# Kernel optimization log

Hardware: AMD Instinct MI355X
Metric: run time of the kernel (lower is better)

Reference implementation:

```python
import jax, jax.numpy as jnp
import numpy as np

N_NODES = 20000
N_EDGES = 160000
FEAT = 512
HEADS = 4
NEG_SLOPE = 0.2


def setup_inputs() -> dict:
    key = jax.random.key(0)
    ks = jax.random.split(key, 8)
    s = 1.0 / np.sqrt(FEAT)
    return {
        "x": jax.random.normal(ks[0], (N_NODES, FEAT), dtype=jnp.float32),
        "edge_index": jax.random.randint(ks[1], (2, N_EDGES), 0, N_NODES, dtype=jnp.int32),
        "W_l": jax.random.normal(ks[2], (FEAT, HEADS * FEAT), dtype=jnp.float32) * s,
        "W_r": jax.random.normal(ks[3], (FEAT, HEADS * FEAT), dtype=jnp.float32) * s,
        "att": jax.random.normal(ks[4], (HEADS, FEAT), dtype=jnp.float32) * s,
        "bias": jax.random.normal(ks[5], (FEAT,), dtype=jnp.float32) * 0.01,
        "W_cls": jax.random.normal(ks[6], (FEAT, 2), dtype=jnp.float32) * s,
        "b_cls": jnp.zeros((2,), dtype=jnp.float32),
    }


def reference(x, edge_index, W_l, W_r, att, bias, W_cls, b_cls):
    N = x.shape[0]
    H, C = att.shape
    # PyG GATv2Conv default: add self-loops
    loops = jnp.arange(N, dtype=edge_index.dtype)
    ei = jnp.concatenate([edge_index, jnp.stack([loops, loops])], axis=1)
    src, dst = ei[0], ei[1]  # message j -> i

    xl = (x @ W_l).reshape(N, H, C)  # source transform
    xr = (x @ W_r).reshape(N, H, C)  # target transform

    # GATv2 score: e_ij = att . LeakyReLU(xl_j + xr_i)   -> [E, H]
    u = xl[src] + xr[dst]                      # [E, H, C]
    e = jnp.einsum('ehc,hc->eh', jax.nn.leaky_relu(u, NEG_SLOPE), att)

    # segment softmax over incoming edges of each dst node
    m = jax.ops.segment_max(e, dst, num_segments=N)          # [N, H]
    alpha = jnp.exp(e - m[dst])
    denom = jax.ops.segment_sum(alpha, dst, num_segments=N)  # [N, H]
    alpha = alpha / denom[dst]

    # aggregate: out_i = sum_j alpha_ij * xl_j
    out = jax.ops.segment_sum(alpha[:, :, None] * xl[src], dst, num_segments=N)  # [N,H,C]
    out = out.mean(axis=1) + bias  # concat=False -> mean over heads, then bias

    return out @ W_cls + b_cls  # [N, num_classes]
```

## Files before the change

kernel.cpp:

```cpp
#include <hip/hip_runtime.h>
#include <hip/hip_bf16.h>

#define FEAT    512
#define HEADS   4
#define NEG     0.2f

typedef unsigned int uint;
typedef unsigned short ushort_t;
typedef __attribute__((ext_vector_type(8))) short bf16x8v;
typedef __attribute__((ext_vector_type(4))) float f32x4v;
typedef __attribute__((ext_vector_type(2))) float f32x2v;
typedef __attribute__((ext_vector_type(4))) uint uint4v;
typedef __attribute__((address_space(3))) uint lds_u32_t;
typedef __attribute__((address_space(1))) const uint g_u32_t;

__device__ inline float bf2f(ushort_t h) { return __uint_as_float(((uint)h) << 16); }
__device__ inline ushort_t f2bf(float f) {
    uint u = __float_as_uint(f);
    u += 0x7fff + ((u >> 16) & 1);
    return (ushort_t)(u >> 16);
}
__device__ inline f32x2v pk_add(f32x2v a, f32x2v b) {
    f32x2v d; asm("v_pk_add_f32 %0, %1, %2" : "=v"(d) : "v"(a), "v"(b)); return d;
}
__device__ inline f32x2v pk_fma(f32x2v a, f32x2v b, f32x2v c) {
    f32x2v d; asm("v_pk_fma_f32 %0, %1, %2, %3" : "=v"(d) : "v"(a), "v"(b), "v"(c)); return d;
}
__device__ inline f32x2v up2v(uint d) {
    f32x2v r; r.x = __uint_as_float(d << 16); r.y = __uint_as_float(d & 0xffff0000u); return r;
}
__device__ inline f32x2v pk_min0(f32x2v a) {
    f32x2v r; r.x = fminf(a.x, 0.f); r.y = fminf(a.y, 0.f); return r;
}

__global__ __launch_bounds__(256) void prep_kernel(
    const ushort_t* __restrict__ xprobe, int* flag,
    int* __restrict__ deg, int N, int NBZ,
    const void* a0, ushort_t* o0, int n0, const void* a1, ushort_t* o1, int n1,
    const void* a2, ushort_t* o2, int n2, const void* a3, ushort_t* o3, int n3,
    const void* __restrict__ Wl, const void* __restrict__ Wr,
    ushort_t* __restrict__ WtL, ushort_t* __restrict__ WtR, int Kk, int HCk) {
    __shared__ int s_isbf;
    __shared__ ushort_t t[64][72];
    int tid = threadIdx.x;
    if (tid < 64) {
        int hits = 0;
        for (int i = tid; i < 128; i += 64) {
            ushort_t w = xprobe[2 * i];
            uint hb = (w >> 8) & 0x7f;
            hits += (hb >= 0x38 && hb <= 0x42) ? 1 : 0;
        }
        #pragma unroll
        for (int off = 32; off >= 1; off >>= 1) hits += __shfl_xor(hits, off);
        if (tid == 0) s_isbf = (hits >= 64) ? 1 : 0;
    }
    __syncthreads();
    int isbf = s_isbf;
    int b = blockIdx.x;
    if (b == 0 && tid == 0) *flag = isbf;

    if (b < NBZ) {
        int i0 = (b * 256 + tid) * 4;
        if (i0 + 4 <= N) *(int4*)&deg[i0] = make_int4(0, 0, 0, 0);
        else for (int j = 0; j < 4; ++j) if (i0 + j < N) deg[i0 + j] = 0;
        return;
    }
    if (b < NBZ + 15) {
        int idx = (b - NBZ) * 256 + tid;
        const void* srcs[4] = {a0, a1, a2, a3};
        ushort_t* dsts[4] = {o0, o1, o2, o3};
        int ns[4] = {n0, n1, n2, n3};
        #pragma unroll
        for (int k = 0; k < 4; ++k) {
            if (idx < ns[k]) {
                dsts[k][idx] = isbf ? ((const ushort_t*)srcs[k])[idx]
                                    : f2bf(((const float*)srcs[k])[idx]);
                return;
            }
            idx -= ns[k];
        }
        return;
    }
    int b2 = b - (NBZ + 15);
    int z = b2 & 1;
    int rest = b2 >> 1;
    int ntk = Kk >> 6;
    int ky = rest % ntk, nxt = rest / ntk;
    const void* in = z ? Wr : Wl;
    ushort_t* outp = z ? WtR : WtL;
    int kt0 = ky * 64, nt0 = nxt * 64;
    int r = tid >> 3;
    int c = (tid & 7) * 8;
    #pragma unroll
    for (int p = 0; p < 2; ++p) {
        int row = r + p * 32;
        size_t base = (size_t)(kt0 + row) * HCk + nt0 + c;
        if (isbf) {
            *(uint4*)&t[row][c] = *(const uint4*)((const ushort_t*)in + base);
        } else {
            const float* f = (const float*)in + base;
            float4 a = *(const float4*)f, bb = *(const float4*)(f + 4);
            ushort_t o[8] = {f2bf(a.x), f2bf(a.y), f2bf(a.z), f2bf(a.w),
                             f2bf(bb.x), f2bf(bb.y), f2bf(bb.z), f2bf(bb.w)};
            *(uint4*)&t[row][c] = *(uint4*)o;
        }
    }
    __syncthreads();
    #pragma unroll
    for (int p = 0; p < 2; ++p) {
        int row = r + p * 32;
        #pragma unroll
        for (int j = 0; j < 8; ++j)
            outp[(size_t)(nt0 + row) * Kk + kt0 + c + j] = t[c + j][row];
    }
}

__global__ __launch_bounds__(256) void histx_kernel(
    const ushort_t* __restrict__ xprobe,
    const int* __restrict__ dstE, int* deg, int E, int NH, int Ngr,
    const void* __restrict__ xin, ushort_t* __restrict__ xc, long long nx) {
    int tid = threadIdx.x;
    int b = blockIdx.x;
    if (b < NH) {
        int i = b * 256 + tid;
        if (i < E) {
            int d = dstE[i];
            if ((uint)d < (uint)Ngr) atomicAdd(&deg[d], 1);
        }
        return;
    }
    __shared__ int s_isbf;
    if (tid < 64) {
        int hits = 0;
        for (int i = tid; i < 128; i += 64) {
            ushort_t w = xprobe[2 * i];
            uint hb = (w >> 8) & 0x7f;
            hits += (hb >= 0x38 && hb <= 0x42) ? 1 : 0;
        }
        #pragma unroll
        for (int off = 32; off >= 1; off >>= 1) hits += __shfl_xor(hits, off);
        if (tid == 0) s_isbf = (hits >= 64) ? 1 : 0;
    }
    __syncthreads();
    if (s_isbf) return;
    long long i0 = ((long long)(b - NH) * 256 + tid) * 8;
    if (i0 + 8 <= nx) {
        const float* f = (const float*)xin + i0;
        float4 a = *(const float4*)f, bb = *(const float4*)(f + 4);
        ushort_t o[8] = {f2bf(a.x), f2bf(a.y), f2bf(a.z), f2bf(a.w),
                         f2bf(bb.x), f2bf(bb.y), f2bf(bb.z), f2bf(bb.w)};
        *(uint4*)&xc[i0] = *(uint4*)o;
    } else {
        for (long long i = i0; i < nx; ++i) xc[i] = f2bf(((const float*)xin)[i]);
    }
}

__global__ __launch_bounds__(256) void scan1(const int* __restrict__ deg, int* __restrict__ part,
                                             int* __restrict__ bsum, int N) {
    __shared__ int tmp[256];
    int b = blockIdx.x, tid = threadIdx.x;
    int i0 = b * 1024 + tid * 4;
    int v[4] = {0, 0, 0, 0};
    if (i0 + 4 <= N) { int4 q = *(const int4*)&deg[i0]; v[0]=q.x+1; v[1]=q.y+1; v[2]=q.z+1; v[3]=q.w+1; }
    else { for (int j = 0; j < 4; ++j) v[j] = (i0 + j < N) ? deg[i0 + j] + 1 : 0; }
    int s0 = v[0], s1 = s0 + v[1], s2 = s1 + v[2], s3 = s2 + v[3];
    tmp[tid] = s3;
    __syncthreads();
    for (int off = 1; off < 256; off <<= 1) {
        int t = (tid >= off) ? tmp[tid - off] : 0;
        __syncthreads();
        tmp[tid] += t;
        __syncthreads();
    }
    int base = tid ? tmp[tid - 1] : 0;
    int e[4] = {base, base + s0, base + s1, base + s2};
    if (i0 + 4 <= N) { *(int4*)&part[i0] = make_int4(e[0], e[1], e[2], e[3]); }
    else { for (int j = 0; j < 4; ++j) if (i0 + j < N) part[i0 + j] = e[j]; }
    if (tid == 255) bsum[b] = tmp[255];
}

__global__ __launch_bounds__(256) void scan3(const int* __restrict__ part, const int* __restrict__ bsum,
                                             int* __restrict__ offsets, int* __restrict__ cursor,
                                             int N, int Nb) {
    __shared__ int s_add, s_tot;
    int b = blockIdx.x, tid = threadIdx.x;
    if (tid < 64) {
        int v = (tid < Nb) ? bsum[tid] : 0;
        int incl = v;
        #pragma unroll
        for (int off = 1; off < 64; off <<= 1) {
            int t = __shfl_up(incl, off);
            if (tid >= off) incl += t;
        }
        if (tid == b) s_add = incl - v;
        if (tid == Nb - 1) s_tot = incl;
    }
    __syncthreads();
    int add = s_add;
    int i0 = b * 1024 + tid * 4;
    #pragma unroll
    for (int j = 0; j < 4; ++j) {
        int i = i0 + j;
        if (i < N) { int o = part[i] + add; offsets[i] = o; cursor[i] = o; }
    }
    if (b == Nb - 1 && tid == 0) offsets[N] = s_tot;
}

__global__ void scatter_kernel(const int* __restrict__ src, const int* __restrict__ dst,
                               int* cursor, int* srcs, int E, int N) {
    int i = blockIdx.x * blockDim.x + threadIdx.x;
    if (i >= E + N) return;
    int s, d;
    if (i < E) { s = src[i]; d = dst[i]; }
    else       { s = i - E; d = i - E; }
    if ((uint)d >= (uint)N) return;
    int pos = atomicAdd(&cursor[d], 1);
    if ((uint)pos < (uint)(E + N)) srcs[pos] = s;
}

__global__ __launch_bounds__(256) void gemm128(const ushort_t* A_bf, const ushort_t* A_cv,
                                               const int* __restrict__ flag,
                                               const ushort_t* __restrict__ Bt,
                                               ushort_t* __restrict__ C,
                                               int M, int Nn, int K, int gyGemm,
                                               const int* __restrict__ esrc,
                                               const int* __restrict__ edst,
                                               int* cursor, int* srcsOut,
                                               int E, int Ngr, int nScB) {
    if ((int)blockIdx.y >= gyGemm) {
        int id = ((int)blockIdx.y - gyGemm) * (int)gridDim.x + (int)blockIdx.x;
        if (id < nScB) {
            int i = id * 256 + (int)threadIdx.x;
            int EN = E + Ngr;
            if (i < EN) {
                int s, d;
                if (i < E) { s = esrc[i]; d = edst[i]; }
                else       { s = i - E; d = i - E; }
                if ((uint)d < (uint)Ngr) {
                    int pos = atomicAdd(&cursor[d], 1);
                    if ((uint)pos < (uint)EN) srcsOut[pos] = s;
                }
            }
        }
        return;
    }
    constexpr int CSTR = 132;
    __shared__ ushort_t SH[128 * CSTR];
    ushort_t* As = SH;
    ushort_t* Bs = SH + 8192;
    const ushort_t* A = (*flag) ? A_bf : A_cv;
    int tid = threadIdx.x;
    int wave = tid >> 6, lane = tid & 63;
    int row0 = blockIdx.y * 128, col0 = blockIdx.x * 128;
    int wm = (wave >> 1) * 64, wn = (wave & 1) * 64;

    f32x4v acc[4][4];
    #pragma unroll
    for (int i = 0; i < 4; ++i)
        #pragma unroll
        for (int j = 0; j < 4; ++j) acc[i][j] = (f32x4v){0.f, 0.f, 0.f, 0.f};

    int fm = lane & 15, kq8 = (lane >> 4) * 8;

    const ushort_t* srcA[2]; ushort_t* dstA0[2]; ushort_t* dstA1[2];
    const ushort_t* srcB[2]; ushort_t* dstB0[2]; ushort_t* dstB1[2];
    #pragma unroll
    for (int i = 0; i < 2; ++i) {
        int p = (wave * 2 + i) * 64 + lane;
        int row = p >> 2, kp = p & 3;
        int gra = row0 + row; if (gra >= M) gra = M - 1;
        srcA[i] = &A[(size_t)gra * K + kp * 8];
        srcB[i] = &Bt[(size_t)(col0 + row) * K + kp * 8];
        dstA0[i] = &As[p * 8]; dstA1[i] = &As[4096 + p * 8];
        dstB0[i] = &Bs[p * 8]; dstB1[i] = &Bs[4096 + p * 8];
    }

    for (int k0 = 0; k0 < K; k0 += 64) {
        #pragma unroll
        for (int i = 0; i < 2; ++i) {
            __builtin_amdgcn_global_load_lds((g_u32_t*)srcA[i],        (lds_u32_t*)dstA0[i], 16, 0, 0);
            __builtin_amdgcn_global_load_lds((g_u32_t*)(srcA[i] + 32), (lds_u32_t*)dstA1[i], 16, 0, 0);
            __builtin_amdgcn_global_load_lds((g_u32_t*)srcB[i],        (lds_u32_t*)dstB0[i], 16, 0, 0);
            __builtin_amdgcn_global_load_lds((g_u32_t*)(srcB[i] + 32), (lds_u32_t*)dstB1[i], 16, 0, 0);
            srcA[i] += 64; srcB[i] += 64;
        }
        __syncthreads();

        #pragma unroll
        for (int panel = 0; panel < 2; ++panel) {
            bf16x8v af[4], bfr[4];
            #pragma unroll
            for (int mi = 0; mi < 4; ++mi)
                af[mi] = *(const bf16x8v*)&As[panel * 4096 + (wm + mi * 16 + fm) * 32 + kq8];
            #pragma unroll
            for (int nj = 0; nj < 4; ++nj)
                bfr[nj] = *(const bf16x8v*)&Bs[panel * 4096 + (wn + nj * 16 + fm) * 32 + kq8];
            #pragma unroll
            for (int mi = 0; mi < 4; ++mi)
                #pragma unroll
                for (int nj = 0; nj < 4; ++nj)
                    acc[mi][nj] = __builtin_amdgcn_mfma_f32_16x16x32_bf16(af[mi], bfr[nj], acc[mi][nj], 0, 0, 0);
        }
        __syncthreads();
    }

    int col = lane & 15, rq = (lane >> 4) * 4;
    #pragma unroll
    for (int mi = 0; mi < 4; ++mi)
        #pragma unroll
        for (int r = 0; r < 4; ++r)
            #pragma unroll
            for (int nj = 0; nj < 4; ++nj)
                SH[(wm + mi * 16 + rq + r) * CSTR + wn + nj * 16 + col] = f2bf(acc[mi][nj][r]);
    __syncthreads();
    #pragma unroll
    for (int j = 0; j < 8; ++j) {
        int base = (tid + j * 256) * 8;
        int r = base >> 7, c = base & 127;
        int gm = row0 + r;
        if (gm < M)
            *(uint4*)&C[(size_t)gm * Nn + col0 + c] = *(const uint4*)&SH[r * CSTR + c];
    }
}

__global__ __launch_bounds__(128, 4) void gat_aggregate(
    const ushort_t* __restrict__ xl, int xl_stride,
    const ushort_t* __restrict__ xr, int xr_stride,
    const int* __restrict__ offsets, const int* __restrict__ srcs,
    const ushort_t* __restrict__ att, const ushort_t* __restrict__ bias,
    const ushort_t* __restrict__ Wc, const ushort_t* __restrict__ bc,
    float* __restrict__ out, int c0, int Cn, int N, int EN) {
    int bn = blockIdx.x;
    if (bn >= Cn) return;
    int n = c0 + bn;
    int tid = threadIdx.x;
    int w = tid >> 6, lane = tid & 63;
    int h = 2 * w + (lane >> 5);
    int r = lane & 31;
    int hoff = h * FEAT + r * 16;

    __shared__ float sh[HEADS][FEAT];
    __shared__ float r0s[2], r1s[2];

    f32x2v xrr[8], attr[8];
    { const uint4v* p = (const uint4v*)&xr[(size_t)bn * xr_stride + hoff];
      uint4v qa = __builtin_nontemporal_load(p);
      uint4v qb = __builtin_nontemporal_load(p + 1);
      xrr[0] = up2v(qa.x); xrr[1] = up2v(qa.y); xrr[2] = up2v(qa.z); xrr[3] = up2v(qa.w);
      xrr[4] = up2v(qb.x); xrr[5] = up2v(qb.y); xrr[6] = up2v(qb.z); xrr[7] = up2v(qb.w); }
    { const ushort_t* p = &att[hoff];
      uint4 qa = *(const uint4*)p, qb = *(const uint4*)(p + 8);
      attr[0] = up2v(qa.x); attr[1] = up2v(qa.y); attr[2] = up2v(qa.z); attr[3] = up2v(qa.w);
      attr[4] = up2v(qb.x); attr[5] = up2v(qb.y); attr[6] = up2v(qb.z); attr[7] = up2v(qb.w); }

    int start = offsets[n], end = offsets[n + 1];
    start = max(0, min(start, EN));
    end   = max(start, min(end, EN));
    int deg = end - start;

    int sv = 0;
    if (lane < deg) sv = srcs[start + lane];

    float l = 0.f;
    f32x2v acc[8] = {{0.f,0.f},{0.f,0.f},{0.f,0.f},{0.f,0.f},
                     {0.f,0.f},{0.f,0.f},{0.f,0.f},{0.f,0.f}};
    const ushort_t* xlh = xl + hoff;
    const f32x2v cneg = {NEG - 1.0f, NEG - 1.0f};

    auto getS = [&](int i) -> int {
        if (i >= deg) i = deg - 1;
        if (i < 0) i = 0;
        int s = (i < 64) ? __shfl(sv, i) : srcs[start + i];
        return ((uint)s >= (uint)N) ? 0 : s;
    };
    auto fetchE = [&](int i, uint4& qa, uint4& qb) {
        int s = getS(i);
        const ushort_t* pp = xlh + (size_t)s * xl_stride;
        qa = *(const uint4*)pp;
        qb = *(const uint4*)(pp + 8);
    };
    auto body = [&](uint4 qa, uint4 qb) {
        f32x2v v[8] = {up2v(qa.x), up2v(qa.y), up2v(qa.z), up2v(qa.w),
                       up2v(qb.x), up2v(qb.y), up2v(qb.z), up2v(qb.w)};
        f32x2v p2 = {0.f, 0.f};
        #pragma unroll
        for (int j = 0; j < 8; ++j) {
            f32x2v u  = pk_add(v[j], xrr[j]);
            f32x2v lr = pk_fma(pk_min0(u), cneg, u);
            p2 = pk_fma(lr, attr[j], p2);
        }
        float p = p2.x + p2.y;
        #pragma unroll
        for (int off = 16; off >= 1; off >>= 1) p += __shfl_xor(p, off);
        float wgt = __expf(p);
        l += wgt;
        f32x2v wv; wv.x = wgt; wv.y = wgt;
        #pragma unroll
        for (int j = 0; j < 8; ++j) acc[j] = pk_fma(wv, v[j], acc[j]);
    };

    uint4 a0q, a0r, a1q, a1r, b0q, b0r, b1q, b1r;
    fetchE(0, a0q, a0r);
    fetchE(1, a1q, a1r);
    for (int e = 0; e < deg; e += 2) {
        fetchE(e + 2, b0q, b0r);
        fetchE(e + 3, b1q, b1r);
        body(a0q, a0r);
        if (e + 1 < deg) body(a1q, a1r);
        a0q = b0q; a0r = b0r; a1q = b1q; a1r = b1r;
    }

    float inv = 0.25f / fmaxf(l, 1e-35f);
    #pragma unroll
    for (int j = 0; j < 8; ++j) {
        sh[h][r * 16 + 2 * j]     = acc[j].x * inv;
        sh[h][r * 16 + 2 * j + 1] = acc[j].y * inv;
    }
    __syncthreads();

    float p0 = 0.f, p1 = 0.f;
    #pragma unroll
    for (int c = tid; c < FEAT; c += 128) {
        float f = sh[0][c] + sh[1][c] + sh[2][c] + sh[3][c] + bf2f(bias[c]);
        uint w2 = *(const uint*)&Wc[c * 2];
        p0 = fmaf(f, bf2f((ushort_t)(w2 & 0xffff)), p0);
        p1 = fmaf(f, bf2f((ushort_t)(w2 >> 16)), p1);
    }
    #pragma unroll
    for (int off = 32; off >= 1; off >>= 1) {
        p0 += __shfl_xor(p0, off);
        p1 += __shfl_xor(p1, off);
    }
    if (lane == 0) { r0s[w] = p0; r1s[w] = p1; }
    __syncthreads();
    if (tid == 0) {
        out[(size_t)n * 2 + 0] = r0s[0] + r0s[1] + bf2f(bc[0]);
        out[(size_t)n * 2 + 1] = r1s[0] + r1s[1] + bf2f(bc[1]);
    }
}

extern "C" void kernel_launch(void* const* d_in, const int* in_sizes, int n_in,
                              void* d_out, int out_size, void* d_ws, size_t ws_size,
                              hipStream_t stream) {
    const void* x    = d_in[0];
    const int*  ei   = (const int*)d_in[1];
    const void* W_l  = d_in[2];
    const void* W_r  = d_in[3];
    const void* att  = d_in[4];
    const void* bias = d_in[5];
    const void* Wc   = d_in[6];
    const void* bc   = d_in[7];
    float* out = (float*)d_out;

    const int N  = in_sizes[0] / FEAT;
    const int E  = in_sizes[1] / 2;
    const int K  = FEAT;
    const int HC = HEADS * FEAT;
    const int EN = E + N;
    const int Nb = (N + 1023) / 1024;

    const int* src = ei;
    const int* dst = ei + E;

    char* base = (char*)d_ws;
    size_t off = 0;
    auto alloc = [&](size_t bytes) -> char* {
        char* p = base + off;
        off = (off + bytes + 255) & ~(size_t)255;
        return p;
    };
    int* flag    = (int*)alloc(4);
    int* offsets = (int*)alloc((size_t)(N + 1) * 4);
    int* cursor  = (int*)alloc((size_t)N * 4);
    int* deg     = (int*)alloc((size_t)N * 4);
    int* part    = (int*)alloc((size_t)N * 4);
    int* bsum    = (int*)alloc((size_t)(Nb + 1) * 4);
    int* srcs    = (int*)alloc((size_t)EN * 4);
    ushort_t* attc  = (ushort_t*)alloc((size_t)HC * 2);
    ushort_t* biasc = (ushort_t*)alloc((size_t)FEAT * 2);
    ushort_t* Wcc   = (ushort_t*)alloc((size_t)FEAT * 2 * 2);
    ushort_t* bcc   = (ushort_t*)alloc(2 * 2);
    ushort_t* xc   = (ushort_t*)alloc((size_t)N * K * 2);
    ushort_t* Wcat = (ushort_t*)alloc((size_t)2 * HC * K * 2);
    size_t fixed = off;

    size_t need_merged = (size_t)N * 2 * HC * 2;
    bool merged = (ws_size >= fixed + need_merged);

    long long NX = (long long)N * K;
    const int NBZ = (N + 1023) / 1024;
    const int nT = (HC / 64) * (K / 64) * 2;
    prep_kernel<<<NBZ + 15 + nT, 256, 0, stream>>>(
        (const ushort_t*)x, flag, deg, N, NBZ,
        att, attc, HC, bias, biasc, FEAT, Wc, Wcc, FEAT * 2, bc, bcc, 2,
        W_l, W_r, Wcat, Wcat + (size_t)HC * K, K, HC);

    const int NH = (E + 255) / 256;
    int nxb = (int)((NX / 8 + 255) / 256);
    histx_kernel<<<NH + nxb, 256, 0, stream>>>(
        (const ushort_t*)x, dst, deg, E, NH, N, x, xc, NX);

    scan1<<<Nb, 256, 0, stream>>>(deg, part, bsum, N);
    scan3<<<Nb, 256, 0, stream>>>(part, bsum, offsets, cursor, N, Nb);

    const ushort_t* x_bf = (const ushort_t*)x;
    const int nScB = (EN + 255) / 256;

    if (merged) {
        ushort_t* xlr = (ushort_t*)(base + fixed);
        int gx = 2 * HC / 128;
        int gyG = (N + 127) / 128;
        int exR = (nScB + gx - 1) / gx;
        dim3 gg(gx, gyG + exR);
        gemm128<<<gg, 256, 0, stream>>>(x_bf, xc, flag, Wcat, xlr, N, 2 * HC, K,
                                        gyG, src, dst, cursor, srcs, E, N, nScB);
        gat_aggregate<<<N, 128, 0, stream>>>(xlr, 2 * HC, xlr + HC, 2 * HC,
                                             offsets, srcs, attc, biasc, Wcc, bcc,
                                             out, 0, N, N, EN);
    } else {
        scatter_kernel<<<nScB, 256, 0, stream>>>(src, dst, cursor, srcs, E, N);
        ushort_t* xl = (ushort_t*)alloc((size_t)N * HC * 2);
        size_t remain = (ws_size > off) ? (ws_size - off) : 0;
        long long Cmax = (long long)(remain / ((size_t)HC * 2));
        int C = (Cmax >= N) ? N : (int)(Cmax & ~63LL);
        if (C < 64) C = 64;
        ushort_t* xrc = (ushort_t*)(base + off);
        ushort_t* Wlt = Wcat;
        ushort_t* Wrt = Wcat + (size_t)HC * K;

        dim3 gl(HC / 128, (N + 127) / 128);
        gemm128<<<gl, 256, 0, stream>>>(x_bf, xc, flag, Wlt, xl, N, HC, K,
                                        (N + 127) / 128, nullptr, nullptr,
                                        nullptr, nullptr, 0, 0, 0);
        for (int c0 = 0; c0 < N; c0 += C) {
            int Cn = (N - c0 < C) ? (N - c0) : C;
            dim3 gr(HC / 128, (Cn + 127) / 128);
            gemm128<<<gr, 256, 0, stream>>>(x_bf + (size_t)c0 * K, xc + (size_t)c0 * K, flag,
                                            Wrt, xrc, Cn, HC, K,
                                            (Cn + 127) / 128, nullptr, nullptr,
                                            nullptr, nullptr, 0, 0, 0);
            gat_aggregate<<<Cn, 128, 0, stream>>>(xl, HC, xrc, HC,
                                                  offsets, srcs, attc, biasc, Wcc, bcc,
                                                  out, c0, Cn, N, EN);
        }
    }
}
```

Before: 320.9 us.

## Fuse prep, degree histogram, and scan into one mega kernel

Replaces four launches (prep, histogram plus x conversion, two-pass scan) with one 1024-thread kernel when N fits in shared memory. Block 0 builds the degree histogram in LDS and does the prefix scan itself, while the other blocks convert the constants, transpose the weights and convert x to bf16. This is meant to remove launch overhead and the global-memory round trips for deg and the partial sums. The cost is that one block serially processes all 160k edges and all 20k nodes, which may become a long critical path.

```diff
diff --git a/kernel.cpp b/kernel.cpp
--- a/kernel.cpp
+++ b/kernel.cpp
@@ -31,6 +31,165 @@
 }
 __device__ inline f32x2v pk_min0(f32x2v a) {
     f32x2v r; r.x = fminf(a.x, 0.f); r.y = fminf(a.y, 0.f); return r;
+}
+
+__global__ __launch_bounds__(1024) void mega_kernel(
+    const ushort_t* __restrict__ xprobe, int* flag,
+    const int* __restrict__ edst, int* __restrict__ offs, int* __restrict__ cur,
+    int N, int E,
+    const void* a0, ushort_t* o0, int n0, const void* a1, ushort_t* o1, int n1,
+    const void* a2, ushort_t* o2, int n2, const void* a3, ushort_t* o3, int n3,
+    const void* __restrict__ Wl, const void* __restrict__ Wr,
+    ushort_t* __restrict__ WtL, ushort_t* __restrict__ WtR,
+    int Kk, int HCk, int nT4b,
+    const void* __restrict__ xin, ushort_t* __restrict__ xc, long long nx) {
+    __shared__ int smem[24576];
+    __shared__ int s_isbf;
+    __shared__ int wtot[16];
+    int tid = threadIdx.x;
+    int b = blockIdx.x;
+
+    if (b == 0) {
+        int* sdeg = smem;
+        for (int i = tid; i < N; i += 1024) sdeg[i] = 0;
+        __syncthreads();
+        int nE4 = E >> 2;
+        for (int i = tid; i < nE4; i += 1024) {
+            int4 q = *(const int4*)&edst[i << 2];
+            if ((uint)q.x < (uint)N) atomicAdd(&sdeg[q.x], 1);
+            if ((uint)q.y < (uint)N) atomicAdd(&sdeg[q.y], 1);
+            if ((uint)q.z < (uint)N) atomicAdd(&sdeg[q.z], 1);
+            if ((uint)q.w < (uint)N) atomicAdd(&sdeg[q.w], 1);
+        }
+        for (int i = (nE4 << 2) + tid; i < E; i += 1024) {
+            int d = edst[i];
+            if ((uint)d < (uint)N) atomicAdd(&sdeg[d], 1);
+        }
+        __syncthreads();
+        int wv = tid >> 6, ln = tid & 63;
+        int seg = (N + 15) >> 4;
+        int sg0 = wv * seg, sg1 = min(sg0 + seg, N);
+        int sum = 0;
+        for (int i = sg0 + ln; i < sg1; i += 64) sum += sdeg[i] + 1;
+        #pragma unroll
+        for (int off = 32; off >= 1; off >>= 1) sum += __shfl_xor(sum, off);
+        if (ln == 0) wtot[wv] = sum;
+        __syncthreads();
+        if (wv == 0) {
+            int v = (ln < 16) ? wtot[ln] : 0;
+            int incl = v;
+            #pragma unroll
+            for (int off = 1; off < 16; off <<= 1) {
+                int t2 = __shfl_up(incl, off);
+                if (ln >= off) incl += t2;
+            }
+            if (ln < 16) wtot[ln] = incl - v;
+            if (ln == 15) offs[N] = incl;
+        }
+        __syncthreads();
+        int carry = wtot[wv];
+        for (int i0 = sg0; i0 < sg1; i0 += 64) {
+            int i = i0 + ln;
+            int v = (i < sg1) ? sdeg[i] + 1 : 0;
+            int incl = v;
+            #pragma unroll
+            for (int off = 1; off < 64; off <<= 1) {
+                int t2 = __shfl_up(incl, off);
+                if (ln >= off) incl += t2;
+            }
+            int excl = carry + incl - v;
+            if (i < sg1) { offs[i] = excl; cur[i] = excl; }
+            carry += __shfl(incl, 63);
+        }
+        return;
+    }
+
+    if (tid < 64) {
+        int hits = 0;
+        for (int i = tid; i < 128; i += 64) {
+            ushort_t w2 = xprobe[2 * i];
+            uint hb = (w2 >> 8) & 0x7f;
+            hits += (hb >= 0x38 && hb <= 0x42) ? 1 : 0;
+        }
+        #pragma unroll
+        for (int off = 32; off >= 1; off >>= 1) hits += __shfl_xor(hits, off);
+        if (tid == 0) s_isbf = (hits >= 64) ? 1 : 0;
+    }
+    __syncthreads();
+    int isbf = s_isbf;
+
+    if (b == 1) {
+        if (tid == 0) *flag = isbf;
+        int total = n0 + n1 + n2 + n3;
+        for (int idx0 = tid; idx0 < total; idx0 += 1024) {
+            int idx = idx0;
+            const void* srcp; ushort_t* dstp;
+            if (idx < n0) { srcp = a0; dstp = o0; }
+            else { idx -= n0;
+              if (idx < n1) { srcp = a1; dstp = o1; }
+              else { idx -= n1;
+                if (idx < n2) { srcp = a2; dstp = o2; }
+                else { idx -= n2; srcp = a3; dstp = o3; } } }
+            dstp[idx] = isbf ? ((const ushort_t*)srcp)[idx]
+                             : f2bf(((const float*)srcp)[idx]);
+        }
+        return;
+    }
+    if (b < 2 + nT4b) {
+        typedef ushort_t t64_t[64][72];
+        t64_t* t4 = (t64_t*)smem;
+        int g = (b - 2) * 4 + (tid >> 8);
+        int sub = tid & 255;
+        int ntk = Kk >> 6;
+        int nTiles = (HCk >> 6) * ntk * 2;
+        int r = sub >> 3;
+        int c = (sub & 7) * 8;
+        ushort_t (*t)[72] = t4[tid >> 8];
+        int z = g & 1;
+        int rest = g >> 1;
+        int ky = rest % ntk, nxt2 = rest / ntk;
+        int kt0 = ky * 64, nt0 = nxt2 * 64;
+        if (g < nTiles) {
+            const void* in = z ? Wr : Wl;
+            #pragma unroll
+            for (int p = 0; p < 2; ++p) {
+                int row = r + p * 32;
+                size_t basei = (size_t)(kt0 + row) * HCk + nt0 + c;
+                if (isbf) {
+                    *(uint4*)&t[row][c] = *(const uint4*)((const ushort_t*)in + basei);
+                } else {
+                    const float* f = (const float*)in + basei;
+                    float4 aa = *(const float4*)f, bb = *(const float4*)(f + 4);
+                    ushort_t o[8] = {f2bf(aa.x), f2bf(aa.y), f2bf(aa.z), f2bf(aa.w),
+                                     f2bf(bb.x), f2bf(bb.y), f2bf(bb.z), f2bf(bb.w)};
+                    *(uint4*)&t[row][c] = *(uint4*)o;
+                }
+            }
+        }
+        __syncthreads();
+        if (g < nTiles) {
+            ushort_t* outp = z ? WtR : WtL;
+            #pragma unroll
+            for (int p = 0; p < 2; ++p) {
+                int row = r + p * 32;
+                #pragma unroll
+                for (int j = 0; j < 8; ++j)
+                    outp[(size_t)(nt0 + row) * Kk + kt0 + c + j] = t[c + j][row];
+            }
+        }
+        return;
+    }
+    if (isbf) return;
+    long long i0 = ((long long)(b - 2 - nT4b) * 1024 + tid) * 8;
+    if (i0 + 8 <= nx) {
+        const float* f = (const float*)xin + i0;
+        float4 aa = *(const float4*)f, bb = *(const float4*)(f + 4);
+        ushort_t o[8] = {f2bf(aa.x), f2bf(aa.y), f2bf(aa.z), f2bf(aa.w),
+                         f2bf(bb.x), f2bf(bb.y), f2bf(bb.z), f2bf(bb.w)};
+        *(uint4*)&xc[i0] = *(uint4*)o;
+    } else {
+        for (long long i = i0; i < nx; ++i) xc[i] = f2bf(((const float*)xin)[i]);
+    }
 }
 
 __global__ __launch_bounds__(256) void prep_kernel(
@@ -394,9 +553,9 @@
         for (int off = 16; off >= 1; off >>= 1) p += __shfl_xor(p, off);
         float wgt = __expf(p);
         l += wgt;
-        f32x2v wv; wv.x = wgt; wv.y = wgt;
-        #pragma unroll
-        for (int j = 0; j < 8; ++j) acc[j] = pk_fma(wv, v[j], acc[j]);
+        f32x2v wv2; wv2.x = wgt; wv2.y = wgt;
+        #pragma unroll
+        for (int j = 0; j < 8; ++j) acc[j] = pk_fma(wv2, v[j], acc[j]);
     };
 
     uint4 a0q, a0r, a1q, a1r, b0q, b0r, b1q, b1r;
@@ -488,20 +647,29 @@
     bool merged = (ws_size >= fixed + need_merged);
 
     long long NX = (long long)N * K;
-    const int NBZ = (N + 1023) / 1024;
-    const int nT = (HC / 64) * (K / 64) * 2;
-    prep_kernel<<<NBZ + 15 + nT, 256, 0, stream>>>(
-        (const ushort_t*)x, flag, deg, N, NBZ,
-        att, attc, HC, bias, biasc, FEAT, Wc, Wcc, FEAT * 2, bc, bcc, 2,
-        W_l, W_r, Wcat, Wcat + (size_t)HC * K, K, HC);
-
-    const int NH = (E + 255) / 256;
-    int nxb = (int)((NX / 8 + 255) / 256);
-    histx_kernel<<<NH + nxb, 256, 0, stream>>>(
-        (const ushort_t*)x, dst, deg, E, NH, N, x, xc, NX);
-
-    scan1<<<Nb, 256, 0, stream>>>(deg, part, bsum, N);
-    scan3<<<Nb, 256, 0, stream>>>(part, bsum, offsets, cursor, N, Nb);
+
+    if (N <= 24576) {
+        int nT4b = ((HC / 64) * (K / 64) * 2 + 3) / 4;
+        int nxb1k = (int)((NX + 8191) / 8192);
+        mega_kernel<<<2 + nT4b + nxb1k, 1024, 0, stream>>>(
+            (const ushort_t*)x, flag, dst, offsets, cursor, N, E,
+            att, attc, HC, bias, biasc, FEAT, Wc, Wcc, FEAT * 2, bc, bcc, 2,
+            W_l, W_r, Wcat, Wcat + (size_t)HC * K, K, HC, nT4b,
+            x, xc, NX);
+    } else {
+        const int NBZ = (N + 1023) / 1024;
+        const int nT = (HC / 64) * (K / 64) * 2;
+        prep_kernel<<<NBZ + 15 + nT, 256, 0, stream>>>(
+            (const ushort_t*)x, flag, deg, N, NBZ,
+            att, attc, HC, bias, biasc, FEAT, Wc, Wcc, FEAT * 2, bc, bcc, 2,
+            W_l, W_r, Wcat, Wcat + (size_t)HC * K, K, HC);
+        const int NH = (E + 255) / 256;
+        int nxb = (int)((NX / 8 + 255) / 256);
+        histx_kernel<<<NH + nxb, 256, 0, stream>>>(
+            (const ushort_t*)x, dst, deg, E, NH, N, x, xc, NX);
+        scan1<<<Nb, 256, 0, stream>>>(deg, part, bsum, N);
+        scan3<<<Nb, 256, 0, stream>>>(part, bsum, offsets, cursor, N, Nb);
+    }
 
     const ushort_t* x_bf = (const ushort_t*)x;
     const int nScB = (EN + 255) / 256;
```

Result: no change. 323.5 us (+0.8%).
